# Kernel optimization log

Measured on AMD Instinct MI355X. Metric: run time of the kernel, lower is better.

## Reference

```python
import jax, jax.numpy as jnp
import numpy as np


def setup_inputs() -> dict:
    key = jax.random.key(0)
    k1, k2 = jax.random.split(key)
    data = jax.random.normal(k1, (16, 64, 128, 128), dtype=jnp.float32)
    weights = jax.random.normal(k2, (128, 64, 3, 3), dtype=jnp.float32)
    return {"data": data, "weights": weights}


def reference(data, weights):
    # Original module performs im2col (unfold+reshape) + matmul, which is
    # mathematically a stride-1 VALID cross-correlation in NCHW layout.
    # weights: [C_out, C_in, kH, kW]; output: [B, C_out, H-kH+1, W-kW+1]
    return jax.lax.conv_general_dilated(
        data, weights,
        window_strides=(1, 1),
        padding="VALID",
        dimension_numbers=("NCHW", "OIHW", "NCHW"),
    )
```

## Files before the change

kernel.cpp:

```cpp
#include <hip/hip_runtime.h>


#define BATCH 16
#define CIN   64
#define HIN   128
#define WIN   128
#define COUT  128
#define HO    126
#define WO    126

typedef short bf16x8 __attribute__((ext_vector_type(8)));
typedef float f32x4  __attribute__((ext_vector_type(4)));

__device__ __forceinline__ unsigned short f2bf(float f) {
    union { float f; unsigned int u; } v; v.f = f;
    unsigned int u = v.u;
    unsigned int r = (u + 0x7fffu + ((u >> 16) & 1u)) >> 16;
    return (unsigned short)r;
}

__device__ __forceinline__ void async16(const void* g, void* l) {
    __builtin_amdgcn_global_load_lds(
        (const __attribute__((address_space(1))) unsigned int*)(unsigned long long)g,
        (__attribute__((address_space(3))) unsigned int*)(unsigned long long)l,
        16, 0, 0);
}

__global__ __launch_bounds__(256) void t1_nchw_to_nhwc(
        const float* __restrict__ x, unsigned short* __restrict__ y) {
    __shared__ unsigned short tile[64 * 68];
    const int b = blockIdx.z, h = blockIdx.y, w0 = blockIdx.x * 64;
    const int t = threadIdx.x;

    const int wl = t & 63, ci0 = t >> 6;
    const float* src = x + (((size_t)b * CIN) * HIN + h) * WIN + w0 + wl;
#pragma unroll
    for (int j = 0; j < 16; j++) {
        const int ci = ci0 + j * 4;
        tile[wl * 68 + ci] = f2bf(src[(size_t)ci * (HIN * WIN)]);
    }
    __syncthreads();

    const int ci4 = (t & 15) * 4, wl2 = t >> 4;
#pragma unroll
    for (int j = 0; j < 4; j++) {
        const int w = wl2 + j * 16;
        ushort4 v = *(const ushort4*)&tile[w * 68 + ci4];
        *(ushort4*)&y[(((size_t)b * HIN + h) * WIN + w0 + w) * CIN + ci4] = v;
    }
}

__global__ __launch_bounds__(256) void t2_weights(
        const float* __restrict__ w, unsigned short* __restrict__ wt) {
    const int idx = blockIdx.x * 256 + threadIdx.x;
    if (idx < COUT * CIN * 9) {
        const int co = idx / (CIN * 9);
        const int r  = idx % (CIN * 9);
        const int ci = r / 9;
        const int k  = r % 9;
        wt[((size_t)k * COUT + co) * CIN + ci] = f2bf(w[idx]);
    }
}

__global__ __launch_bounds__(512, 2) void conv_mfma(
        const unsigned short* __restrict__ nhwc,
        const unsigned short* __restrict__ wt,
        float* __restrict__ out) {
    __shared__ __align__(16) char smem[49408 + 32768];
    short* Bs = (short*)smem;
    short* As = (short*)(smem + 49408);

    const int raw = blockIdx.y * 126 + blockIdx.x;
    const int s = (raw & 7) * 252 + (raw >> 3);
    const int b = s / 126;
    const int oh = s - b * 126;

    const int tid  = threadIdx.x;
    const int lane = tid & 63, wid = tid >> 6;
    const int co0  = (wid & 3) * 32;
    const int wn   = wid >> 1 & 0;
    const int spn  = wid >> 2;
    const int col  = lane & 15, quad = lane >> 4;
    const int swl = (lane * 16) ^ ((lane >> 3) << 4);

    {
        const char* src = (const char*)nhwc + (size_t)(b * HIN + oh) * (WIN * CIN * 2);
        char* dst = (char*)Bs;
#pragma unroll
        for (int i = 0; i < 6; i++) {
            const int c = wid * 6 + i;
            async16(src + c * 1024 + swl, dst + c * 1024 + lane * 16);
        }
    }
    {
        const char* srcA = (const char*)wt;
        char* dstA = (char*)As;
#pragma unroll
        for (int i = 0; i < 2; i++) {
            const int c = wid * 2 + i;
            async16(srcA + c * 1024 + swl, dstA + c * 1024 + lane * 16);
        }
    }
    __syncthreads();

    f32x4 acc[2][4] = {};

#pragma unroll
    for (int t = 0; t < 9; t++) {
        const int kh = t / 3, kw = t - kh * 3;

        if (t + 1 < 9) {
            const char* srcA = (const char*)wt + (size_t)(t + 1) * 16384;
            char* dstA = (char*)As + ((t + 1) & 1) * 16384;
#pragma unroll
            for (int i = 0; i < 2; i++) {
                const int c = wid * 2 + i;
                async16(srcA + c * 1024 + swl, dstA + c * 1024 + lane * 16);
            }
        }

        const short* At = As + (t & 1) * 8192;
#pragma unroll
        for (int kk = 0; kk < 2; kk++) {
            bf16x8 aa[2], bb[4];
#pragma unroll
            for (int mi = 0; mi < 2; mi++) {
                const int r = co0 + mi * 16 + col;
                aa[mi] = *(const bf16x8*)&At[(r * 64 + kk * 32 + quad * 8) ^ ((r & 7) << 3)];
            }
#pragma unroll
            for (int ni = 0; ni < 4; ni++) {
                const int r = kh * 128 + spn * 64 + ni * 16 + col + kw;
                bb[ni] = *(const bf16x8*)&Bs[(r * 64 + kk * 32 + quad * 8) ^ ((r & 7) << 3)];
            }
#pragma unroll
            for (int mi = 0; mi < 2; mi++)
#pragma unroll
                for (int ni = 0; ni < 4; ni++)
                    acc[mi][ni] = __builtin_amdgcn_mfma_f32_16x16x32_bf16(
                        aa[mi], bb[ni], acc[mi][ni], 0, 0, 0);
        }
        if (t + 1 < 9) __syncthreads();
    }

#pragma unroll
    for (int ni = 0; ni < 4; ni++) {
        const int ow = spn * 64 + ni * 16 + col;
        if (ow < WO) {
#pragma unroll
            for (int mi = 0; mi < 2; mi++) {
                const int co = co0 + mi * 16 + quad * 4;
                float* o = out + (((size_t)b * COUT + co) * HO + oh) * WO + ow;
#pragma unroll
                for (int r = 0; r < 4; r++)
                    o[(size_t)r * HO * WO] = acc[mi][ni][r];
            }
        }
    }
}

__global__ __launch_bounds__(256) void conv_direct(
        const float* __restrict__ x, const float* __restrict__ w,
        float* __restrict__ y) {
    const int idx = blockIdx.x * 256 + threadIdx.x;
    if (idx >= BATCH * COUT * HO * WO) return;
    const int ow = idx % WO;
    int t = idx / WO;
    const int oh = t % HO; t /= HO;
    const int co = t % COUT;
    const int b  = t / COUT;
    float acc = 0.f;
    const float* xb = x + (((size_t)b * CIN) * HIN + oh) * WIN + ow;
    const float* wc = w + (size_t)co * (CIN * 9);
    for (int ci = 0; ci < CIN; ci++) {
#pragma unroll
        for (int kh = 0; kh < 3; kh++)
#pragma unroll
            for (int kw = 0; kw < 3; kw++)
                acc += xb[(size_t)ci * (HIN * WIN) + kh * WIN + kw] * wc[ci * 9 + kh * 3 + kw];
    }
    y[idx] = acc;
}

extern "C" void kernel_launch(void* const* d_in, const int* in_sizes, int n_in,
                              void* d_out, int out_size, void* d_ws, size_t ws_size,
                              hipStream_t stream) {
    const float* data    = (const float*)d_in[0];
    const float* weights = (const float*)d_in[1];
    float* out = (float*)d_out;

    const size_t nhwc_bytes = (size_t)BATCH * HIN * WIN * CIN * 2;
    const size_t slack = 4096;
    const size_t wt_bytes = (size_t)9 * COUT * CIN * 2;
    const size_t need = nhwc_bytes + slack + wt_bytes;

    if (ws_size >= need) {
        unsigned short* nhwc = (unsigned short*)d_ws;
        unsigned short* wt   = (unsigned short*)((char*)d_ws + nhwc_bytes + slack);
        t1_nchw_to_nhwc<<<dim3(2, HIN, BATCH), 256, 0, stream>>>(data, nhwc);
        t2_weights<<<(COUT * CIN * 9 + 255) / 256, 256, 0, stream>>>(weights, wt);
        conv_mfma<<<dim3(126, BATCH), 512, 0, stream>>>(nhwc, wt, out);
    } else {
        const int n = BATCH * COUT * HO * WO;
        conv_direct<<<(n + 255) / 256, 256, 0, stream>>>(data, weights, out);
    }
}
```

Baseline: 244.6 us.

## Fuse NCHW-to-NHWC bf16 conversion into conv kernel with half-row tiles

Drops the separate transpose kernel and its bf16 NHWC workspace. Each block now reads the three fp32 input rows directly for its 64-wide half output row, converts them to bf16 and transposes them through LDS into a swizzled halo buffer. The grid doubles to two blocks per output row, with a smaller per-block MFMA tile and launch bounds that allow more resident blocks. The cost is that neighbouring blocks reread and reconvert overlapping input rows, and the halo build adds extra barriers before the MFMA loop.

```diff
diff --git a/kernel.cpp b/kernel.cpp
--- a/kernel.cpp
+++ b/kernel.cpp
@@ -24,30 +24,6 @@
         (const __attribute__((address_space(1))) unsigned int*)(unsigned long long)g,
         (__attribute__((address_space(3))) unsigned int*)(unsigned long long)l,
         16, 0, 0);
-}
-
-__global__ __launch_bounds__(256) void t1_nchw_to_nhwc(
-        const float* __restrict__ x, unsigned short* __restrict__ y) {
-    __shared__ unsigned short tile[64 * 68];
-    const int b = blockIdx.z, h = blockIdx.y, w0 = blockIdx.x * 64;
-    const int t = threadIdx.x;
-
-    const int wl = t & 63, ci0 = t >> 6;
-    const float* src = x + (((size_t)b * CIN) * HIN + h) * WIN + w0 + wl;
-#pragma unroll
-    for (int j = 0; j < 16; j++) {
-        const int ci = ci0 + j * 4;
-        tile[wl * 68 + ci] = f2bf(src[(size_t)ci * (HIN * WIN)]);
-    }
-    __syncthreads();
-
-    const int ci4 = (t & 15) * 4, wl2 = t >> 4;
-#pragma unroll
-    for (int j = 0; j < 4; j++) {
-        const int w = wl2 + j * 16;
-        ushort4 v = *(const ushort4*)&tile[w * 68 + ci4];
-        *(ushort4*)&y[(((size_t)b * HIN + h) * WIN + w0 + w) * CIN + ci4] = v;
-    }
 }
 
 __global__ __launch_bounds__(256) void t2_weights(
@@ -62,36 +38,29 @@
     }
 }
 
-__global__ __launch_bounds__(512, 2) void conv_mfma(
-        const unsigned short* __restrict__ nhwc,
+__global__ __launch_bounds__(512, 4) void conv_fused(
+        const float* __restrict__ x,
         const unsigned short* __restrict__ wt,
         float* __restrict__ out) {
-    __shared__ __align__(16) char smem[49408 + 32768];
-    short* Bs = (short*)smem;
-    short* As = (short*)(smem + 49408);
-
-    const int raw = blockIdx.y * 126 + blockIdx.x;
-    const int s = (raw & 7) * 252 + (raw >> 3);
-    const int b = s / 126;
-    const int oh = s - b * 126;
+    __shared__ __align__(16) char smem[26112 + 32768 + 9520];
+    short* halo = (short*)smem;
+    short* As   = (short*)(smem + 26112);
+    unsigned short* tile = (unsigned short*)(smem + 26112 + 32768);
+
+    const int raw = (blockIdx.z * 126 + blockIdx.y) * 2 + blockIdx.x;
+    const int s = (raw & 7) * 504 + (raw >> 3);
+    const int b  = s / 252;
+    const int r2 = s - b * 252;
+    const int oh = r2 >> 1;
+    const int W0 = (r2 & 1) * 64;
 
     const int tid  = threadIdx.x;
     const int lane = tid & 63, wid = tid >> 6;
     const int co0  = (wid & 3) * 32;
-    const int wn   = wid >> 1 & 0;
-    const int spn  = wid >> 2;
+    const int n0   = (wid >> 2) * 32;
     const int col  = lane & 15, quad = lane >> 4;
     const int swl = (lane * 16) ^ ((lane >> 3) << 4);
 
-    {
-        const char* src = (const char*)nhwc + (size_t)(b * HIN + oh) * (WIN * CIN * 2);
-        char* dst = (char*)Bs;
-#pragma unroll
-        for (int i = 0; i < 6; i++) {
-            const int c = wid * 6 + i;
-            async16(src + c * 1024 + swl, dst + c * 1024 + lane * 16);
-        }
-    }
     {
         const char* srcA = (const char*)wt;
         char* dstA = (char*)As;
@@ -101,14 +70,45 @@
             async16(srcA + c * 1024 + swl, dstA + c * 1024 + lane * 16);
         }
     }
-    __syncthreads();
-
-    f32x4 acc[2][4] = {};
+
+    for (int kh = 0; kh < 3; kh++) {
+        const int h = oh + kh;
+        {
+            const int w4 = (tid & 15) * 4, cib = tid >> 4;
+#pragma unroll
+            for (int j = 0; j < 2; j++) {
+                const int ci = cib + 32 * j;
+                f32x4 v = *(const f32x4*)&x[(((size_t)b * CIN + ci) * HIN + h) * WIN + W0 + w4];
+#pragma unroll
+                for (int q = 0; q < 4; q++)
+                    tile[(w4 + q) * 70 + ci] = f2bf(v[q]);
+            }
+            if (W0 == 0 && tid < 256) {
+                const int w = 64 + (tid & 3), ci = tid >> 2;
+                tile[w * 70 + ci] = f2bf(x[(((size_t)b * CIN + ci) * HIN + h) * WIN + w]);
+            }
+        }
+        __syncthreads();
+        {
+            const int ci4 = (tid & 15) * 4, wr = tid >> 4;
+#pragma unroll
+            for (int jj = 0; jj < 3; jj++) {
+                const int widx = wr + 32 * jj;
+                if (jj < 2 || wr < 4) {
+                    ushort4 v = *(const ushort4*)&tile[widx * 70 + ci4];
+                    const int r = kh * 68 + widx;
+                    *(ushort4*)((char*)halo + ((r * 128 + ci4 * 2) ^ ((r & 7) << 4))) = v;
+                }
+            }
+        }
+        __syncthreads();
+    }
+
+    f32x4 acc[2][2] = {};
 
 #pragma unroll
     for (int t = 0; t < 9; t++) {
         const int kh = t / 3, kw = t - kh * 3;
-
         if (t + 1 < 9) {
             const char* srcA = (const char*)wt + (size_t)(t + 1) * 16384;
             char* dstA = (char*)As + ((t + 1) & 1) * 16384;
@@ -118,25 +118,24 @@
                 async16(srcA + c * 1024 + swl, dstA + c * 1024 + lane * 16);
             }
         }
-
         const short* At = As + (t & 1) * 8192;
 #pragma unroll
         for (int kk = 0; kk < 2; kk++) {
-            bf16x8 aa[2], bb[4];
+            bf16x8 aa[2], bb[2];
 #pragma unroll
             for (int mi = 0; mi < 2; mi++) {
                 const int r = co0 + mi * 16 + col;
                 aa[mi] = *(const bf16x8*)&At[(r * 64 + kk * 32 + quad * 8) ^ ((r & 7) << 3)];
             }
 #pragma unroll
-            for (int ni = 0; ni < 4; ni++) {
-                const int r = kh * 128 + spn * 64 + ni * 16 + col + kw;
-                bb[ni] = *(const bf16x8*)&Bs[(r * 64 + kk * 32 + quad * 8) ^ ((r & 7) << 3)];
+            for (int ni = 0; ni < 2; ni++) {
+                const int r = kh * 68 + n0 + ni * 16 + col + kw;
+                bb[ni] = *(const bf16x8*)&halo[(r * 64 + kk * 32 + quad * 8) ^ ((r & 7) << 3)];
             }
 #pragma unroll
             for (int mi = 0; mi < 2; mi++)
 #pragma unroll
-                for (int ni = 0; ni < 4; ni++)
+                for (int ni = 0; ni < 2; ni++)
                     acc[mi][ni] = __builtin_amdgcn_mfma_f32_16x16x32_bf16(
                         aa[mi], bb[ni], acc[mi][ni], 0, 0, 0);
         }
@@ -144,8 +143,8 @@
     }
 
 #pragma unroll
-    for (int ni = 0; ni < 4; ni++) {
-        const int ow = spn * 64 + ni * 16 + col;
+    for (int ni = 0; ni < 2; ni++) {
+        const int ow = W0 + n0 + ni * 16 + col;
         if (ow < WO) {
 #pragma unroll
             for (int mi = 0; mi < 2; mi++) {
@@ -189,17 +188,12 @@
     const float* weights = (const float*)d_in[1];
     float* out = (float*)d_out;
 
-    const size_t nhwc_bytes = (size_t)BATCH * HIN * WIN * CIN * 2;
-    const size_t slack = 4096;
     const size_t wt_bytes = (size_t)9 * COUT * CIN * 2;
-    const size_t need = nhwc_bytes + slack + wt_bytes;
-
-    if (ws_size >= need) {
-        unsigned short* nhwc = (unsigned short*)d_ws;
-        unsigned short* wt   = (unsigned short*)((char*)d_ws + nhwc_bytes + slack);
-        t1_nchw_to_nhwc<<<dim3(2, HIN, BATCH), 256, 0, stream>>>(data, nhwc);
+
+    if (ws_size >= wt_bytes) {
+        unsigned short* wt = (unsigned short*)d_ws;
         t2_weights<<<(COUT * CIN * 9 + 255) / 256, 256, 0, stream>>>(weights, wt);
-        conv_mfma<<<dim3(126, BATCH), 512, 0, stream>>>(nhwc, wt, out);
+        conv_fused<<<dim3(2, 126, BATCH), 512, 0, stream>>>(data, wt, out);
     } else {
         const int n = BATCH * COUT * HO * WO;
         conv_direct<<<(n + 255) / 256, 256, 0, stream>>>(data, weights, out);
```

After: 237.9 us. 1.03x faster.
